# Optimization experiments

Hardware: AMD Instinct MI355X
Metric: run time of the kernel (lower is better)

The kernel has to match this reference:

```python
import jax, jax.numpy as jnp
import numpy as np

P, B, I, O = 32, 512, 1024, 1024


def setup_inputs() -> dict:
    key = jax.random.key(0)
    kx, kw = jax.random.split(key)
    # strictly {0,1}-valued binary tensors stored as float32, as in the torch module
    x = (jax.random.uniform(kx, (P, B, I)) > 0.5).astype(jnp.float32)
    w = (jax.random.uniform(kw, (2, P, I, O)) > 0.5).astype(jnp.float32)
    return {"x": x, "w": w}


def reference(x, w):
    # x: [P, B, I] binary; w: [2, P, I, O] binary.
    # out = x @ W0 + (~x) @ W1  (logical_not of a {0,1} float is 1 - x)
    notx = 1.0 - x
    out = jnp.einsum('pbi,pio->pbo', x, w[0]) + jnp.einsum('pbi,pio->pbo', notx, w[1])
    return out  # [P, B, O], activation == 'none'
```

## Files before the change

### kernel.cpp

```cpp
#include <hip/hip_runtime.h>


namespace {

constexpr int PP = 32;
constexpr int BB = 512;
constexpr int II = 1024;
constexpr int OO = 1024;

constexpr int BM = 256;
constexpr int BN = 256;
constexpr int BK = 32;

constexpr int KPA = 40;

__device__ __forceinline__ int boff(int o, int k) {
    return o * 40 + (o >> 2) * 8 + k;
}

typedef __attribute__((ext_vector_type(8))) short bf16x8;
typedef __attribute__((ext_vector_type(4))) float f32x4;

constexpr int A_BYTES = BM * KPA * 2;
constexpr int B_BYTES = (BN * 40 + (BN / 4) * 8) * 2;
constexpr int SMEM_BYTES = A_BYTES + B_BYTES;

__device__ __forceinline__ unsigned pk2(float lo, float hi) {
    return (__float_as_uint(lo) >> 16) | (__float_as_uint(hi) & 0xFFFF0000u);
}

__global__ __launch_bounds__(1024) void ebl_kernel(const float* __restrict__ x,
                                                   const float* __restrict__ w,
                                                   float* __restrict__ out) {
    __shared__ __align__(16) char smem[SMEM_BYTES];
    unsigned short* As = (unsigned short*)smem;
    unsigned short* Bs = (unsigned short*)(smem + A_BYTES);
    float* Scr    = (float*)smem;
    float* ColSum = (float*)(smem + 16384);

    const int t  = (int)threadIdx.x;
    const int l  = t & 63;
    const int wv = t >> 6;
    const int wm = wv & 3;
    const int wn = wv >> 2;
    const int lq = l >> 4;
    const int ln = l & 15;

    const int p  = (int)blockIdx.z;
    const int b0 = (int)blockIdx.y * BM;
    const int o0 = (int)blockIdx.x * BN;

    const float* xp  = x + ((size_t)p * BB + b0) * II;
    const float* w0p = w + (size_t)p * II * OO;
    const float* w1p = w + (size_t)(PP + p) * II * OO;

    const int a_row = t >> 3;
    const int a_col = (t & 7) * 4;
    const int b_colg = 4 * l;

    int a_rd[4], b_rd[4];
#pragma unroll
    for (int mt = 0; mt < 4; ++mt)
        a_rd[mt] = (wm * 64 + mt * 16 + ln) * KPA + lq * 8;
#pragma unroll
    for (int nt = 0; nt < 4; ++nt)
        b_rd[nt] = boff(wn * 64 + nt * 16 + ln, lq * 8);

    f32x4 acc[4][4];
#pragma unroll
    for (int mt = 0; mt < 4; ++mt)
#pragma unroll
        for (int nt = 0; nt < 4; ++nt)
            acc[mt][nt] = (f32x4){0.f, 0.f, 0.f, 0.f};

    f32x4 csum = (f32x4){0.f, 0.f, 0.f, 0.f};

    const float* xa0  = xp + (size_t)a_row * II + a_col;
    const float* xa1  = xp + (size_t)(a_row + 128) * II + a_col;
    const float* wb00 = w0p + (size_t)(2 * wv) * OO + o0 + b_colg;
    const float* wb01 = w0p + (size_t)(2 * wv + 1) * OO + o0 + b_colg;
    const float* wb10 = w1p + (size_t)(2 * wv) * OO + o0 + b_colg;
    const float* wb11 = w1p + (size_t)(2 * wv + 1) * OO + o0 + b_colg;

    for (int kk = 0; kk < II; kk += BK) {
        f32x4 a0  = *(const f32x4*)(xa0 + kk);
        f32x4 a1  = *(const f32x4*)(xa1 + kk);
        f32x4 p00 = *(const f32x4*)(wb00 + (size_t)kk * OO);
        f32x4 p01 = *(const f32x4*)(wb01 + (size_t)kk * OO);
        f32x4 p10 = *(const f32x4*)(wb10 + (size_t)kk * OO);
        f32x4 p11 = *(const f32x4*)(wb11 + (size_t)kk * OO);

        __syncthreads();

        *(uint2*)(&As[a_row * KPA + a_col]) =
            make_uint2(pk2(a0.x, a0.y), pk2(a0.z, a0.w));
        *(uint2*)(&As[(a_row + 128) * KPA + a_col]) =
            make_uint2(pk2(a1.x, a1.y), pk2(a1.z, a1.w));

        f32x4 d0 = p00 - p10;
        f32x4 d1 = p01 - p11;
        csum += p10;
        csum += p11;
        const int kloc = 2 * wv;
#pragma unroll
        for (int c = 0; c < 4; ++c)
            *(unsigned*)(&Bs[boff(b_colg + c, kloc)]) = pk2(d0[c], d1[c]);

        __syncthreads();

        bf16x8 af[4], bfm[4];
#pragma unroll
        for (int mt = 0; mt < 4; ++mt)
            af[mt] = *(const bf16x8*)(&As[a_rd[mt]]);
#pragma unroll
        for (int nt = 0; nt < 4; ++nt)
            bfm[nt] = *(const bf16x8*)(&Bs[b_rd[nt]]);
#pragma unroll
        for (int mt = 0; mt < 4; ++mt)
#pragma unroll
            for (int nt = 0; nt < 4; ++nt)
                acc[mt][nt] = __builtin_amdgcn_mfma_f32_16x16x32_bf16(
                    af[mt], bfm[nt], acc[mt][nt], 0, 0, 0);
    }

    __syncthreads();
    *(f32x4*)(&Scr[wv * 256 + l * 4]) = csum;
    __syncthreads();
    if (t < 256) {
        float s = 0.f;
#pragma unroll
        for (int ww = 0; ww < 16; ++ww) s += Scr[ww * 256 + t];
        ColSum[t] = s;
    }
    __syncthreads();

    float* op = out + (size_t)p * BB * OO + o0;
#pragma unroll
    for (int nt = 0; nt < 4; ++nt) {
        const int ocol = wn * 64 + nt * 16 + ln;
        const float cs = ColSum[ocol];
#pragma unroll
        for (int mt = 0; mt < 4; ++mt) {
            const int row = b0 + wm * 64 + mt * 16 + lq * 4;
#pragma unroll
            for (int r = 0; r < 4; ++r)
                op[(size_t)(row + r) * OO + ocol] = acc[mt][nt][r] + cs;
        }
    }
}

}

extern "C" void kernel_launch(void* const* d_in, const int* in_sizes, int n_in,
                              void* d_out, int out_size, void* d_ws, size_t ws_size,
                              hipStream_t stream) {
    const float* x = (const float*)d_in[0];
    const float* w = (const float*)d_in[1];
    float* out = (float*)d_out;
    dim3 grid(OO / BN, BB / BM, PP);
    ebl_kernel<<<grid, dim3(1024, 1, 1), 0, stream>>>(x, w, out);
}
```

Baseline: 443.1 us.

## Shrink GEMM tile to 128x128 with 256-thread blocks for more concurrent blocks

Reduces the block tile from 256x256 with 1024 threads to 128x128 with 256 threads (4 waves, each still computing 64x64), and sets launch bounds to allow 3 blocks per CU. Each thread now loads four x rows and four weight vectors per k-step, and the global-to-LDS mapping and column-sum reduction are rebuilt for the smaller tile. The aim is more blocks in the grid and per CU (512 vs 128 blocks on 256 CUs), better load balance and latency hiding. The cost is more global re-reads of x and w because each block reuses less data.

```diff
diff --git a/kernel.cpp b/kernel.cpp
--- a/kernel.cpp
+++ b/kernel.cpp
@@ -8,8 +8,8 @@
 constexpr int II = 1024;
 constexpr int OO = 1024;
 
-constexpr int BM = 256;
-constexpr int BN = 256;
+constexpr int BM = 128;
+constexpr int BN = 128;
 constexpr int BK = 32;
 
 constexpr int KPA = 40;
@@ -29,20 +29,20 @@
     return (__float_as_uint(lo) >> 16) | (__float_as_uint(hi) & 0xFFFF0000u);
 }
 
-__global__ __launch_bounds__(1024) void ebl_kernel(const float* __restrict__ x,
-                                                   const float* __restrict__ w,
-                                                   float* __restrict__ out) {
+__global__ __launch_bounds__(256, 3) void ebl_kernel(const float* __restrict__ x,
+                                                     const float* __restrict__ w,
+                                                     float* __restrict__ out) {
     __shared__ __align__(16) char smem[SMEM_BYTES];
     unsigned short* As = (unsigned short*)smem;
     unsigned short* Bs = (unsigned short*)(smem + A_BYTES);
     float* Scr    = (float*)smem;
-    float* ColSum = (float*)(smem + 16384);
+    float* ColSum = (float*)(smem + 4096);
 
     const int t  = (int)threadIdx.x;
     const int l  = t & 63;
     const int wv = t >> 6;
-    const int wm = wv & 3;
-    const int wn = wv >> 2;
+    const int wm = wv & 1;
+    const int wn = wv >> 1;
     const int lq = l >> 4;
     const int ln = l & 15;
 
@@ -51,12 +51,14 @@
     const int o0 = (int)blockIdx.x * BN;
 
     const float* xp  = x + ((size_t)p * BB + b0) * II;
-    const float* w0p = w + (size_t)p * II * OO;
-    const float* w1p = w + (size_t)(PP + p) * II * OO;
+    const float* w0p = w + (size_t)p * II * OO + o0;
+    const float* w1p = w + (size_t)(PP + p) * II * OO + o0;
 
-    const int a_row = t >> 3;
-    const int a_col = (t & 7) * 4;
-    const int b_colg = 4 * l;
+    const int ar = t >> 3;
+    const int ac = (t & 7) * 4;
+    const int kp = t >> 5;
+    const int bc = (t & 31) * 4;
+    const int k0 = 2 * kp;
 
     int a_rd[4], b_rd[4];
 #pragma unroll
@@ -75,36 +77,47 @@
 
     f32x4 csum = (f32x4){0.f, 0.f, 0.f, 0.f};
 
-    const float* xa0  = xp + (size_t)a_row * II + a_col;
-    const float* xa1  = xp + (size_t)(a_row + 128) * II + a_col;
-    const float* wb00 = w0p + (size_t)(2 * wv) * OO + o0 + b_colg;
-    const float* wb01 = w0p + (size_t)(2 * wv + 1) * OO + o0 + b_colg;
-    const float* wb10 = w1p + (size_t)(2 * wv) * OO + o0 + b_colg;
-    const float* wb11 = w1p + (size_t)(2 * wv + 1) * OO + o0 + b_colg;
+    const float* xa  = xp + (size_t)ar * II + ac;
+    const float* wa0 = w0p + (size_t)k0 * OO + bc;
+    const float* wa1 = w1p + (size_t)k0 * OO + bc;
 
     for (int kk = 0; kk < II; kk += BK) {
-        f32x4 a0  = *(const f32x4*)(xa0 + kk);
-        f32x4 a1  = *(const f32x4*)(xa1 + kk);
-        f32x4 p00 = *(const f32x4*)(wb00 + (size_t)kk * OO);
-        f32x4 p01 = *(const f32x4*)(wb01 + (size_t)kk * OO);
-        f32x4 p10 = *(const f32x4*)(wb10 + (size_t)kk * OO);
-        f32x4 p11 = *(const f32x4*)(wb11 + (size_t)kk * OO);
+        f32x4 a0 = *(const f32x4*)(xa + kk);
+        f32x4 a1 = *(const f32x4*)(xa + 32 * II + kk);
+        f32x4 a2 = *(const f32x4*)(xa + 64 * II + kk);
+        f32x4 a3 = *(const f32x4*)(xa + 96 * II + kk);
+        const float* w0k = wa0 + (size_t)kk * OO;
+        const float* w1k = wa1 + (size_t)kk * OO;
+        f32x4 p00 = *(const f32x4*)(w0k);
+        f32x4 p01 = *(const f32x4*)(w0k + OO);
+        f32x4 p02 = *(const f32x4*)(w0k + 16 * OO);
+        f32x4 p03 = *(const f32x4*)(w0k + 17 * OO);
+        f32x4 p10 = *(const f32x4*)(w1k);
+        f32x4 p11 = *(const f32x4*)(w1k + OO);
+        f32x4 p12 = *(const f32x4*)(w1k + 16 * OO);
+        f32x4 p13 = *(const f32x4*)(w1k + 17 * OO);
 
         __syncthreads();
 
-        *(uint2*)(&As[a_row * KPA + a_col]) =
+        *(uint2*)(&As[ar * KPA + ac]) =
             make_uint2(pk2(a0.x, a0.y), pk2(a0.z, a0.w));
-        *(uint2*)(&As[(a_row + 128) * KPA + a_col]) =
+        *(uint2*)(&As[(ar + 32) * KPA + ac]) =
             make_uint2(pk2(a1.x, a1.y), pk2(a1.z, a1.w));
+        *(uint2*)(&As[(ar + 64) * KPA + ac]) =
+            make_uint2(pk2(a2.x, a2.y), pk2(a2.z, a2.w));
+        *(uint2*)(&As[(ar + 96) * KPA + ac]) =
+            make_uint2(pk2(a3.x, a3.y), pk2(a3.z, a3.w));
 
         f32x4 d0 = p00 - p10;
         f32x4 d1 = p01 - p11;
-        csum += p10;
-        csum += p11;
-        const int kloc = 2 * wv;
+        f32x4 d2 = p02 - p12;
+        f32x4 d3 = p03 - p13;
+        csum += p10; csum += p11; csum += p12; csum += p13;
 #pragma unroll
-        for (int c = 0; c < 4; ++c)
-            *(unsigned*)(&Bs[boff(b_colg + c, kloc)]) = pk2(d0[c], d1[c]);
+        for (int c = 0; c < 4; ++c) {
+            *(unsigned*)(&Bs[boff(bc + c, k0)])      = pk2(d0[c], d1[c]);
+            *(unsigned*)(&Bs[boff(bc + c, k0 + 16)]) = pk2(d2[c], d3[c]);
+        }
 
         __syncthreads();
 
@@ -124,12 +137,12 @@
     }
 
     __syncthreads();
-    *(f32x4*)(&Scr[wv * 256 + l * 4]) = csum;
+    *(f32x4*)(&Scr[kp * 128 + bc]) = csum;
     __syncthreads();
-    if (t < 256) {
+    if (t < 128) {
         float s = 0.f;
 #pragma unroll
-        for (int ww = 0; ww < 16; ++ww) s += Scr[ww * 256 + t];
+        for (int g = 0; g < 8; ++g) s += Scr[g * 128 + t];
         ColSum[t] = s;
     }
     __syncthreads();
@@ -158,5 +171,5 @@
     const float* w = (const float*)d_in[1];
     float* out = (float*)d_out;
     dim3 grid(OO / BN, BB / BM, PP);
-    ebl_kernel<<<grid, dim3(1024, 1, 1), 0, stream>>>(x, w, out);
+    ebl_kernel<<<grid, dim3(256, 1, 1), 0, stream>>>(x, w, out);
 }
```

Result: slower. 459.3 us (+3.7%).

## Split into bf16 prep pass and direct-to-LDS swizzled GEMM kernel

Applied to the files above, without the earlier changes.

Adds a prep kernel that converts x to bf16, builds a transposed bf16 weight-difference matrix (W0-W1), and computes the W1 column sums into workspace. The GEMM kernel then streams the bf16 operands straight into swizzled LDS with global_load_lds, using 128x128 tiles, 256 threads and BK=64. The aim is to stop re-reading and re-converting the fp32 weights in every block and to halve GEMM operand traffic. In exchange it adds a second launch and a workspace write/read round trip, and the GEMM loop is single-buffered with no overlap between loads and compute.

```diff
diff --git a/kernel.cpp b/kernel.cpp
--- a/kernel.cpp
+++ b/kernel.cpp
@@ -8,63 +8,126 @@
 constexpr int II = 1024;
 constexpr int OO = 1024;
 
-constexpr int BM = 256;
-constexpr int BN = 256;
-constexpr int BK = 32;
-
-constexpr int KPA = 40;
-
-__device__ __forceinline__ int boff(int o, int k) {
-    return o * 40 + (o >> 2) * 8 + k;
-}
-
 typedef __attribute__((ext_vector_type(8))) short bf16x8;
 typedef __attribute__((ext_vector_type(4))) float f32x4;
-
-constexpr int A_BYTES = BM * KPA * 2;
-constexpr int B_BYTES = (BN * 40 + (BN / 4) * 8) * 2;
-constexpr int SMEM_BYTES = A_BYTES + B_BYTES;
 
 __device__ __forceinline__ unsigned pk2(float lo, float hi) {
     return (__float_as_uint(lo) >> 16) | (__float_as_uint(hi) & 0xFFFF0000u);
 }
 
-__global__ __launch_bounds__(1024) void ebl_kernel(const float* __restrict__ x,
+__global__ __launch_bounds__(256, 2) void ebl_prep(const float* __restrict__ x,
                                                    const float* __restrict__ w,
+                                                   unsigned short* __restrict__ dWT,
+                                                   unsigned short* __restrict__ xbf,
+                                                   float* __restrict__ colsum) {
+    const int t = (int)threadIdx.x;
+    const int bid = (int)blockIdx.x;
+
+    if (bid < 256) {
+        const int p  = bid >> 3;
+        const int o0 = (bid & 7) * 128;
+        const int og = t & 31;
+        const int kg = t >> 5;
+        const int o  = o0 + 4 * og;
+        const float* w0p = w + (size_t)p * (II * OO) + o;
+        const float* w1p = w + (size_t)(PP + p) * (II * OO) + o;
+
+        float cs0 = 0.f, cs1 = 0.f, cs2 = 0.f, cs3 = 0.f;
+
+        for (int it = 0; it < 16; ++it) {
+            const int kb = 64 * it + 8 * kg;
+            const float* r0 = w0p + (size_t)kb * OO;
+            const float* r1 = w1p + (size_t)kb * OO;
+            f32x4 q0[8], q1[8];
+#pragma unroll
+            for (int j = 0; j < 8; ++j) q0[j] = *(const f32x4*)(r0 + (size_t)j * OO);
+#pragma unroll
+            for (int j = 0; j < 8; ++j) q1[j] = *(const f32x4*)(r1 + (size_t)j * OO);
+
+#pragma unroll
+            for (int c = 0; c < 4; ++c) {
+                uint4 st;
+                st.x = pk2(q0[0][c] - q1[0][c], q0[1][c] - q1[1][c]);
+                st.y = pk2(q0[2][c] - q1[2][c], q0[3][c] - q1[3][c]);
+                st.z = pk2(q0[4][c] - q1[4][c], q0[5][c] - q1[5][c]);
+                st.w = pk2(q0[6][c] - q1[6][c], q0[7][c] - q1[7][c]);
+                *(uint4*)(&dWT[((size_t)p * OO + o + c) * II + kb]) = st;
+            }
+#pragma unroll
+            for (int j = 0; j < 8; ++j) {
+                cs0 += q1[j].x; cs1 += q1[j].y; cs2 += q1[j].z; cs3 += q1[j].w;
+            }
+        }
+
+        __shared__ float Scr[8 * 128];
+        *(f32x4*)(&Scr[kg * 128 + 4 * og]) = (f32x4){cs0, cs1, cs2, cs3};
+        __syncthreads();
+        if (t < 128) {
+            float s = 0.f;
+#pragma unroll
+            for (int g = 0; g < 8; ++g) s += Scr[g * 128 + t];
+            colsum[p * OO + o0 + t] = s;
+        }
+    } else {
+        const size_t base = (size_t)(bid - 256) * 65536;
+        for (int it = 0; it < 16; ++it) {
+#pragma unroll
+            for (int j = 0; j < 4; ++j) {
+                const size_t idx = base + (size_t)it * 4096 + j * 1024 + 4 * t;
+                f32x4 v = *(const f32x4*)(x + idx);
+                *(uint2*)(&xbf[idx]) = make_uint2(pk2(v.x, v.y), pk2(v.z, v.w));
+            }
+        }
+    }
+}
+
+__device__ __forceinline__ void load_lds16(const unsigned short* g, unsigned short* l) {
+    __builtin_amdgcn_global_load_lds(
+        (const __attribute__((address_space(1))) unsigned int*)g,
+        (__attribute__((address_space(3))) unsigned int*)l, 16, 0, 0);
+}
+
+__global__ __launch_bounds__(256, 3) void ebl_gemm(const unsigned short* __restrict__ xbf,
+                                                   const unsigned short* __restrict__ dWT,
+                                                   const float* __restrict__ colsum,
                                                    float* __restrict__ out) {
-    __shared__ __align__(16) char smem[SMEM_BYTES];
-    unsigned short* As = (unsigned short*)smem;
-    unsigned short* Bs = (unsigned short*)(smem + A_BYTES);
-    float* Scr    = (float*)smem;
-    float* ColSum = (float*)(smem + 16384);
+    __shared__ __align__(16) unsigned short As[128 * 64];
+    __shared__ __align__(16) unsigned short Bs[128 * 64];
 
     const int t  = (int)threadIdx.x;
     const int l  = t & 63;
     const int wv = t >> 6;
-    const int wm = wv & 3;
-    const int wn = wv >> 2;
+    const int wm = wv & 1;
+    const int wn = wv >> 1;
     const int lq = l >> 4;
     const int ln = l & 15;
 
     const int p  = (int)blockIdx.z;
-    const int b0 = (int)blockIdx.y * BM;
-    const int o0 = (int)blockIdx.x * BN;
+    const int b0 = (int)blockIdx.y * 128;
+    const int o0 = (int)blockIdx.x * 128;
 
-    const float* xp  = x + ((size_t)p * BB + b0) * II;
-    const float* w0p = w + (size_t)p * II * OO;
-    const float* w1p = w + (size_t)(PP + p) * II * OO;
+    const unsigned short* Ag = xbf + ((size_t)p * BB + b0) * II;
+    const unsigned short* Bg = dWT + ((size_t)p * OO + o0) * II;
 
-    const int a_row = t >> 3;
-    const int a_col = (t & 7) * 4;
-    const int b_colg = 4 * l;
+    const int ri = l >> 3, sj = l & 7;
+    int gof[4], lbase[4];
+#pragma unroll
+    for (int q = 0; q < 4; ++q) {
+        const int r0  = 8 * (4 * wv + q);
+        const int row = r0 + ri;
+        gof[q]   = row * II + 8 * (sj ^ (row & 7));
+        lbase[q] = r0 * 64;
+    }
 
-    int a_rd[4], b_rd[4];
+    int aoff[2][4], boff[2][4];
 #pragma unroll
-    for (int mt = 0; mt < 4; ++mt)
-        a_rd[mt] = (wm * 64 + mt * 16 + ln) * KPA + lq * 8;
+    for (int s = 0; s < 2; ++s)
 #pragma unroll
-    for (int nt = 0; nt < 4; ++nt)
-        b_rd[nt] = boff(wn * 64 + nt * 16 + ln, lq * 8);
+        for (int mt = 0; mt < 4; ++mt) {
+            const int j = 8 * ((4 * s + lq) ^ (ln & 7));
+            aoff[s][mt] = (wm * 64 + mt * 16 + ln) * 64 + j;
+            boff[s][mt] = (wn * 64 + mt * 16 + ln) * 64 + j;
+        }
 
     f32x4 acc[4][4];
 #pragma unroll
@@ -73,78 +136,46 @@
         for (int nt = 0; nt < 4; ++nt)
             acc[mt][nt] = (f32x4){0.f, 0.f, 0.f, 0.f};
 
-    f32x4 csum = (f32x4){0.f, 0.f, 0.f, 0.f};
-
-    const float* xa0  = xp + (size_t)a_row * II + a_col;
-    const float* xa1  = xp + (size_t)(a_row + 128) * II + a_col;
-    const float* wb00 = w0p + (size_t)(2 * wv) * OO + o0 + b_colg;
-    const float* wb01 = w0p + (size_t)(2 * wv + 1) * OO + o0 + b_colg;
-    const float* wb10 = w1p + (size_t)(2 * wv) * OO + o0 + b_colg;
-    const float* wb11 = w1p + (size_t)(2 * wv + 1) * OO + o0 + b_colg;
-
-    for (int kk = 0; kk < II; kk += BK) {
-        f32x4 a0  = *(const f32x4*)(xa0 + kk);
-        f32x4 a1  = *(const f32x4*)(xa1 + kk);
-        f32x4 p00 = *(const f32x4*)(wb00 + (size_t)kk * OO);
-        f32x4 p01 = *(const f32x4*)(wb01 + (size_t)kk * OO);
-        f32x4 p10 = *(const f32x4*)(wb10 + (size_t)kk * OO);
-        f32x4 p11 = *(const f32x4*)(wb11 + (size_t)kk * OO);
-
+    for (int kk = 0; kk < II; kk += 64) {
+#pragma unroll
+        for (int q = 0; q < 4; ++q) {
+            load_lds16(Ag + gof[q] + kk, As + lbase[q]);
+            load_lds16(Bg + gof[q] + kk, Bs + lbase[q]);
+        }
         __syncthreads();
 
-        *(uint2*)(&As[a_row * KPA + a_col]) =
-            make_uint2(pk2(a0.x, a0.y), pk2(a0.z, a0.w));
-        *(uint2*)(&As[(a_row + 128) * KPA + a_col]) =
-            make_uint2(pk2(a1.x, a1.y), pk2(a1.z, a1.w));
-
-        f32x4 d0 = p00 - p10;
-        f32x4 d1 = p01 - p11;
-        csum += p10;
-        csum += p11;
-        const int kloc = 2 * wv;
 #pragma unroll
-        for (int c = 0; c < 4; ++c)
-            *(unsigned*)(&Bs[boff(b_colg + c, kloc)]) = pk2(d0[c], d1[c]);
-
+        for (int s = 0; s < 2; ++s) {
+            bf16x8 af[4], bfv[4];
+#pragma unroll
+            for (int mt = 0; mt < 4; ++mt) af[mt] = *(const bf16x8*)(As + aoff[s][mt]);
+#pragma unroll
+            for (int nt = 0; nt < 4; ++nt) bfv[nt] = *(const bf16x8*)(Bs + boff[s][nt]);
+#pragma unroll
+            for (int mt = 0; mt < 4; ++mt)
+#pragma unroll
+                for (int nt = 0; nt < 4; ++nt)
+                    acc[mt][nt] = __builtin_amdgcn_mfma_f32_16x16x32_bf16(
+                        af[mt], bfv[nt], acc[mt][nt], 0, 0, 0);
+        }
         __syncthreads();
-
-        bf16x8 af[4], bfm[4];
-#pragma unroll
-        for (int mt = 0; mt < 4; ++mt)
-            af[mt] = *(const bf16x8*)(&As[a_rd[mt]]);
-#pragma unroll
-        for (int nt = 0; nt < 4; ++nt)
-            bfm[nt] = *(const bf16x8*)(&Bs[b_rd[nt]]);
-#pragma unroll
-        for (int mt = 0; mt < 4; ++mt)
-#pragma unroll
-            for (int nt = 0; nt < 4; ++nt)
-                acc[mt][nt] = __builtin_amdgcn_mfma_f32_16x16x32_bf16(
-                    af[mt], bfm[nt], acc[mt][nt], 0, 0, 0);
     }
 
-    __syncthreads();
-    *(f32x4*)(&Scr[wv * 256 + l * 4]) = csum;
-    __syncthreads();
-    if (t < 256) {
-        float s = 0.f;
+    float cs[4];
 #pragma unroll
-        for (int ww = 0; ww < 16; ++ww) s += Scr[ww * 256 + t];
-        ColSum[t] = s;
-    }
-    __syncthreads();
+    for (int nt = 0; nt < 4; ++nt)
+        cs[nt] = colsum[p * OO + o0 + wn * 64 + nt * 16 + ln];
 
-    float* op = out + (size_t)p * BB * OO + o0;
+    float* op = out + ((size_t)p * BB + b0) * OO + o0;
 #pragma unroll
     for (int nt = 0; nt < 4; ++nt) {
         const int ocol = wn * 64 + nt * 16 + ln;
-        const float cs = ColSum[ocol];
 #pragma unroll
         for (int mt = 0; mt < 4; ++mt) {
-            const int row = b0 + wm * 64 + mt * 16 + lq * 4;
+            const int row = wm * 64 + mt * 16 + lq * 4;
 #pragma unroll
             for (int r = 0; r < 4; ++r)
-                op[(size_t)(row + r) * OO + ocol] = acc[mt][nt][r] + cs;
+                op[(size_t)(row + r) * OO + ocol] = acc[mt][nt][r] + cs[nt];
         }
     }
 }
@@ -157,6 +188,12 @@
     const float* x = (const float*)d_in[0];
     const float* w = (const float*)d_in[1];
     float* out = (float*)d_out;
-    dim3 grid(OO / BN, BB / BM, PP);
-    ebl_kernel<<<grid, dim3(1024, 1, 1), 0, stream>>>(x, w, out);
+
+    unsigned short* dWT = (unsigned short*)d_ws;
+    unsigned short* xbf = (unsigned short*)((char*)d_ws + (64u << 20));
+    float* colsum = (float*)((char*)d_ws + (96u << 20));
+
+    ebl_prep<<<dim3(512, 1, 1), dim3(256, 1, 1), 0, stream>>>(x, w, dWT, xbf, colsum);
+    ebl_gemm<<<dim3(OO / 128, BB / 128, PP), dim3(256, 1, 1), 0, stream>>>(
+        xbf, dWT, colsum, out);
 }
```

Measured after the change: 483.4 us. 1.09x slower.

## Drop LDS staging and load MFMA fragments directly from global memory

Applied to the files above, without the earlier changes.

Removes shared-memory tiles and all barriers. Each wave now loads its x and w fragments straight from global memory into registers in MFMA layout, and computes the W1 column sums with wave shuffles. Blocks become 512 threads covering all 512 batch rows by 64 output columns. The bf16 packing switches to a perm instruction. The trade is that each wave reloads the same B fragments, and the w loads are strided scalar column reads (8 rows per lane), so cross-wave reuse through LDS is lost and global/L2 traffic goes up.

```diff
diff --git a/kernel.cpp b/kernel.cpp
--- a/kernel.cpp
+++ b/kernel.cpp
@@ -8,63 +8,35 @@
 constexpr int II = 1024;
 constexpr int OO = 1024;
 
-constexpr int BM = 256;
-constexpr int BN = 256;
-constexpr int BK = 32;
-
-constexpr int KPA = 40;
-
-__device__ __forceinline__ int boff(int o, int k) {
-    return o * 40 + (o >> 2) * 8 + k;
-}
-
 typedef __attribute__((ext_vector_type(8))) short bf16x8;
 typedef __attribute__((ext_vector_type(4))) float f32x4;
 
-constexpr int A_BYTES = BM * KPA * 2;
-constexpr int B_BYTES = (BN * 40 + (BN / 4) * 8) * 2;
-constexpr int SMEM_BYTES = A_BYTES + B_BYTES;
-
 __device__ __forceinline__ unsigned pk2(float lo, float hi) {
-    return (__float_as_uint(lo) >> 16) | (__float_as_uint(hi) & 0xFFFF0000u);
+    return __builtin_amdgcn_perm(__float_as_uint(hi), __float_as_uint(lo),
+                                 0x07060302u);
 }
 
-__global__ __launch_bounds__(1024) void ebl_kernel(const float* __restrict__ x,
-                                                   const float* __restrict__ w,
-                                                   float* __restrict__ out) {
-    __shared__ __align__(16) char smem[SMEM_BYTES];
-    unsigned short* As = (unsigned short*)smem;
-    unsigned short* Bs = (unsigned short*)(smem + A_BYTES);
-    float* Scr    = (float*)smem;
-    float* ColSum = (float*)(smem + 16384);
+union BF8 {
+    unsigned u[4];
+    bf16x8 v;
+};
 
+__global__ __launch_bounds__(512, 2) void ebl_kernel(const float* __restrict__ x,
+                                                     const float* __restrict__ w,
+                                                     float* __restrict__ out) {
     const int t  = (int)threadIdx.x;
     const int l  = t & 63;
     const int wv = t >> 6;
-    const int wm = wv & 3;
-    const int wn = wv >> 2;
     const int lq = l >> 4;
     const int ln = l & 15;
 
-    const int p  = (int)blockIdx.z;
-    const int b0 = (int)blockIdx.y * BM;
-    const int o0 = (int)blockIdx.x * BN;
+    const int p  = (int)blockIdx.y;
+    const int o0 = (int)blockIdx.x * 64;
+    const int m0 = wv * 64;
 
-    const float* xp  = x + ((size_t)p * BB + b0) * II;
-    const float* w0p = w + (size_t)p * II * OO;
-    const float* w1p = w + (size_t)(PP + p) * II * OO;
-
-    const int a_row = t >> 3;
-    const int a_col = (t & 7) * 4;
-    const int b_colg = 4 * l;
-
-    int a_rd[4], b_rd[4];
-#pragma unroll
-    for (int mt = 0; mt < 4; ++mt)
-        a_rd[mt] = (wm * 64 + mt * 16 + ln) * KPA + lq * 8;
-#pragma unroll
-    for (int nt = 0; nt < 4; ++nt)
-        b_rd[nt] = boff(wn * 64 + nt * 16 + ln, lq * 8);
+    const float* xa = x + ((size_t)p * BB + m0 + ln) * II + 8 * lq;
+    const float* wb0 = w + (size_t)p * II * OO + (size_t)(8 * lq) * OO + o0 + ln;
+    const float* wb1 = wb0 + (size_t)PP * II * OO;
 
     f32x4 acc[4][4];
 #pragma unroll
@@ -73,80 +45,68 @@
         for (int nt = 0; nt < 4; ++nt)
             acc[mt][nt] = (f32x4){0.f, 0.f, 0.f, 0.f};
 
-    f32x4 csum = (f32x4){0.f, 0.f, 0.f, 0.f};
+    float cs[4] = {0.f, 0.f, 0.f, 0.f};
 
-    const float* xa0  = xp + (size_t)a_row * II + a_col;
-    const float* xa1  = xp + (size_t)(a_row + 128) * II + a_col;
-    const float* wb00 = w0p + (size_t)(2 * wv) * OO + o0 + b_colg;
-    const float* wb01 = w0p + (size_t)(2 * wv + 1) * OO + o0 + b_colg;
-    const float* wb10 = w1p + (size_t)(2 * wv) * OO + o0 + b_colg;
-    const float* wb11 = w1p + (size_t)(2 * wv + 1) * OO + o0 + b_colg;
+#pragma unroll 2
+    for (int kk = 0; kk < II; kk += 32) {
+        BF8 af[4];
+#pragma unroll
+        for (int mt = 0; mt < 4; ++mt) {
+            const float* ap = xa + (size_t)(mt * 16) * II + kk;
+            f32x4 lo = *(const f32x4*)ap;
+            f32x4 hi = *(const f32x4*)(ap + 4);
+            af[mt].u[0] = pk2(lo.x, lo.y);
+            af[mt].u[1] = pk2(lo.z, lo.w);
+            af[mt].u[2] = pk2(hi.x, hi.y);
+            af[mt].u[3] = pk2(hi.z, hi.w);
+        }
 
-    for (int kk = 0; kk < II; kk += BK) {
-        f32x4 a0  = *(const f32x4*)(xa0 + kk);
-        f32x4 a1  = *(const f32x4*)(xa1 + kk);
-        f32x4 p00 = *(const f32x4*)(wb00 + (size_t)kk * OO);
-        f32x4 p01 = *(const f32x4*)(wb01 + (size_t)kk * OO);
-        f32x4 p10 = *(const f32x4*)(wb10 + (size_t)kk * OO);
-        f32x4 p11 = *(const f32x4*)(wb11 + (size_t)kk * OO);
+#pragma unroll
+        for (int nt = 0; nt < 4; ++nt) {
+            const float* b0p = wb0 + (size_t)kk * OO + nt * 16;
+            const float* b1p = wb1 + (size_t)kk * OO + nt * 16;
+            float q0[8], q1[8];
+#pragma unroll
+            for (int j = 0; j < 8; ++j) q0[j] = b0p[(size_t)j * OO];
+#pragma unroll
+            for (int j = 0; j < 8; ++j) q1[j] = b1p[(size_t)j * OO];
 
-        __syncthreads();
-
-        *(uint2*)(&As[a_row * KPA + a_col]) =
-            make_uint2(pk2(a0.x, a0.y), pk2(a0.z, a0.w));
-        *(uint2*)(&As[(a_row + 128) * KPA + a_col]) =
-            make_uint2(pk2(a1.x, a1.y), pk2(a1.z, a1.w));
-
-        f32x4 d0 = p00 - p10;
-        f32x4 d1 = p01 - p11;
-        csum += p10;
-        csum += p11;
-        const int kloc = 2 * wv;
+            float d[8];
 #pragma unroll
-        for (int c = 0; c < 4; ++c)
-            *(unsigned*)(&Bs[boff(b_colg + c, kloc)]) = pk2(d0[c], d1[c]);
-
-        __syncthreads();
-
-        bf16x8 af[4], bfm[4];
+            for (int j = 0; j < 8; ++j) {
+                d[j] = q0[j] - q1[j];
+                cs[nt] += q1[j];
+            }
+            BF8 bf;
+            bf.u[0] = pk2(d[0], d[1]);
+            bf.u[1] = pk2(d[2], d[3]);
+            bf.u[2] = pk2(d[4], d[5]);
+            bf.u[3] = pk2(d[6], d[7]);
 #pragma unroll
-        for (int mt = 0; mt < 4; ++mt)
-            af[mt] = *(const bf16x8*)(&As[a_rd[mt]]);
-#pragma unroll
-        for (int nt = 0; nt < 4; ++nt)
-            bfm[nt] = *(const bf16x8*)(&Bs[b_rd[nt]]);
-#pragma unroll
-        for (int mt = 0; mt < 4; ++mt)
-#pragma unroll
-            for (int nt = 0; nt < 4; ++nt)
+            for (int mt = 0; mt < 4; ++mt)
                 acc[mt][nt] = __builtin_amdgcn_mfma_f32_16x16x32_bf16(
-                    af[mt], bfm[nt], acc[mt][nt], 0, 0, 0);
+                    af[mt].v, bf.v, acc[mt][nt], 0, 0, 0);
+        }
     }
 
-    __syncthreads();
-    *(f32x4*)(&Scr[wv * 256 + l * 4]) = csum;
-    __syncthreads();
-    if (t < 256) {
-        float s = 0.f;
-#pragma unroll
-        for (int ww = 0; ww < 16; ++ww) s += Scr[ww * 256 + t];
-        ColSum[t] = s;
-    }
-    __syncthreads();
-
-    float* op = out + (size_t)p * BB * OO + o0;
 #pragma unroll
     for (int nt = 0; nt < 4; ++nt) {
-        const int ocol = wn * 64 + nt * 16 + ln;
-        const float cs = ColSum[ocol];
+        cs[nt] += __shfl_xor(cs[nt], 16);
+        cs[nt] += __shfl_xor(cs[nt], 32);
+    }
+
+    float* op = out + ((size_t)p * BB + m0) * OO + o0;
 #pragma unroll
-        for (int mt = 0; mt < 4; ++mt) {
-            const int row = b0 + wm * 64 + mt * 16 + lq * 4;
+    for (int mt = 0; mt < 4; ++mt)
 #pragma unroll
-            for (int r = 0; r < 4; ++r)
-                op[(size_t)(row + r) * OO + ocol] = acc[mt][nt][r] + cs;
+        for (int nt = 0; nt < 4; ++nt) {
+            const int col = nt * 16 + ln;
+#pragma unroll
+            for (int r = 0; r < 4; ++r) {
+                const int row = mt * 16 + lq * 4 + r;
+                op[(size_t)row * OO + col] = acc[mt][nt][r] + cs[nt];
+            }
         }
-    }
 }
 
 }
@@ -157,6 +117,6 @@
     const float* x = (const float*)d_in[0];
     const float* w = (const float*)d_in[1];
     float* out = (float*)d_out;
-    dim3 grid(OO / BN, BB / BM, PP);
-    ebl_kernel<<<grid, dim3(1024, 1, 1), 0, stream>>>(x, w, out);
+    dim3 grid(OO / 64, PP, 1);
+    ebl_kernel<<<grid, dim3(512, 1, 1), 0, stream>>>(x, w, out);
 }
```

New measurement: 593.0 us. +33.8%, slower.
